# Performance work log

Hardware: AMD Instinct MI355X
Metric: run time of the kernel (lower is better)

## Reference

```python
import jax, jax.numpy as jnp
import numpy as np

N_NODES = 50000
N_EDGES = 800000
D_IN = 100
HID = 128
N_LAYERS = 3
N_GRAPHS = 64


def setup_inputs() -> dict:
    key = jax.random.key(0)
    ks = jax.random.split(key, 10)
    x = jax.random.normal(ks[0], (N_NODES, D_IN), dtype=jnp.float32)
    edge_index = jax.random.randint(ks[1], (2, N_EDGES), 0, N_NODES, dtype=jnp.int64)
    batch = jnp.sort(jax.random.randint(ks[2], (N_NODES,), 0, N_GRAPHS, dtype=jnp.int64))
    s = 1.0 / np.sqrt(D_IN)
    W_enc = jax.random.uniform(ks[3], (D_IN, HID), jnp.float32, -s, s)
    b_enc = jax.random.uniform(ks[4], (HID,), jnp.float32, -s, s)
    sh = 1.0 / np.sqrt(HID)
    gcn_W = jax.random.uniform(ks[5], (N_LAYERS, HID, HID), jnp.float32, -sh, sh)
    gcn_b = jax.random.uniform(ks[6], (N_LAYERS, HID), jnp.float32, -sh, sh)
    W_reg = jax.random.uniform(ks[7], (HID, 1), jnp.float32, -sh, sh)
    b_reg = jax.random.uniform(ks[8], (1,), jnp.float32, -sh, sh)
    return {"x": x, "edge_index": edge_index, "batch": batch,
            "W_enc": W_enc, "b_enc": b_enc, "gcn_W": gcn_W, "gcn_b": gcn_b,
            "W_reg": W_reg, "b_reg": b_reg}


def reference(x, edge_index, batch, W_enc, b_enc, gcn_W, gcn_b, W_reg, b_reg):
    N = x.shape[0]
    # node encoder
    h = x @ W_enc + b_enc  # [N, HID]
    # GCN normalization with self-loops (edge_weight = 1, PyG gcn_norm)
    loop = jnp.arange(N, dtype=edge_index.dtype)
    src = jnp.concatenate([edge_index[0], loop])  # [E+N]
    dst = jnp.concatenate([edge_index[1], loop])
    deg = jax.ops.segment_sum(jnp.ones_like(src, dtype=h.dtype), dst, num_segments=N)
    dinv = jnp.where(deg > 0, jax.lax.rsqrt(deg), 0.0)
    norm = dinv[src] * dinv[dst]  # [E+N]
    for i in range(N_LAYERS):
        m = (h @ gcn_W[i])[src] * norm[:, None]           # gather + scale messages
        h = jax.ops.segment_sum(m, dst, num_segments=N)   # scatter-add aggregate
        h = jax.nn.relu(h + gcn_b[i])
    # global mean pool over graphs
    sums = jax.ops.segment_sum(h, batch, num_segments=N_GRAPHS)
    cnt = jax.ops.segment_sum(jnp.ones((N,), dtype=h.dtype), batch, num_segments=N_GRAPHS)
    pooled = sums / jnp.maximum(cnt, 1.0)[:, None]        # [N_GRAPHS, HID]
    return pooled @ W_reg + b_reg                         # [N_GRAPHS, 1]
```

## Files before the change

kernel.cpp:

```cpp
#include <hip/hip_runtime.h>
#include <hip/hip_fp16.h>

#define N_NODES 50000
#define N_EDGES 800000
#define D_INN 100
#define HID 128
#define N_GRAPHS 64
#define NBLK ((N_NODES + 255) / 256)
#define POOL_ROWS 128
#define POOL_BLOCKS ((N_NODES + POOL_ROWS - 1) / POOL_ROWS)

#define NBUCK 8
#define NODES_PER_BUCK (N_NODES / NBUCK)
#define SCAT_BLOCKS 2048
#define GEMM_BLOCKS 512
#define N_CHUNK (N_NODES / 16)

typedef _Float16 f16x8 __attribute__((ext_vector_type(8)));
typedef _Float16 f16x4 __attribute__((ext_vector_type(4)));
typedef float f32x4 __attribute__((ext_vector_type(4)));

__global__ __launch_bounds__(256) void k_setup(int* __restrict__ deg,
                                               float* __restrict__ sums,
                                               const float* __restrict__ W,
                                               const float* __restrict__ We,
                                               __half* __restrict__ Wt,
                                               __half* __restrict__ Wte) {
    int i = blockIdx.x * 256 + threadIdx.x;
    if (i < N_NODES) deg[i] = 1;
    if (i < N_GRAPHS * HID) sums[i] = 0.f;
    if (i < 3 * HID * HID) {
        int l = i >> 14, rem = i & 16383;
        int c = rem >> 7, k = rem & 127;
        Wt[(l << 14) + c * HID + k] = __float2half(W[(l << 14) + k * HID + c]);
    } else if (i < 4 * HID * HID) {
        int j = i - 3 * HID * HID;
        int c = j >> 7, k = j & 127;
        float v = (k < D_INN) ? We[k * HID + c] : 0.f;
        Wte[c * HID + k] = __float2half(v);
    }
}

__global__ __launch_bounds__(256) void k_deg(const int* __restrict__ dst,
                                             int* __restrict__ deg) {
    int b = blockIdx.x & (NBUCK - 1);
    int lo = b * NODES_PER_BUCK, hi = lo + NODES_PER_BUCK;
    int sub = blockIdx.x >> 3, nsub = gridDim.x >> 3;
    for (int e = sub * 256 + threadIdx.x; e < N_EDGES; e += nsub * 256) {
        int d = dst[e];
        if (d >= lo && d < hi) atomicAdd(&deg[d], 1);
    }
}

__global__ __launch_bounds__(256) void k_scan1(const int* __restrict__ deg,
                                               int* __restrict__ incl,
                                               int* __restrict__ bsums) {
    __shared__ int sm[256];
    int i = blockIdx.x * 256 + threadIdx.x;
    int v = (i < N_NODES) ? deg[i] : 0;
    sm[threadIdx.x] = v;
    __syncthreads();
    for (int off = 1; off < 256; off <<= 1) {
        int t = (threadIdx.x >= off) ? sm[threadIdx.x - off] : 0;
        __syncthreads();
        sm[threadIdx.x] += t;
        __syncthreads();
    }
    if (i < N_NODES) incl[i] = sm[threadIdx.x];
    if (threadIdx.x == 255) bsums[blockIdx.x] = sm[255];
}

__global__ __launch_bounds__(256) void k_scan2(const int* __restrict__ bsums,
                                               int* __restrict__ boff) {
    __shared__ int sm[256];
    int v = (threadIdx.x < NBLK) ? bsums[threadIdx.x] : 0;
    sm[threadIdx.x] = v;
    __syncthreads();
    for (int off = 1; off < 256; off <<= 1) {
        int t = (threadIdx.x >= off) ? sm[threadIdx.x - off] : 0;
        __syncthreads();
        sm[threadIdx.x] += t;
        __syncthreads();
    }
    boff[threadIdx.x] = sm[threadIdx.x] - v;
}

__global__ void k_scan3(const int* __restrict__ incl, const int* __restrict__ boff,
                        const int* __restrict__ deg, int* __restrict__ offsets,
                        int* __restrict__ cursor, int* __restrict__ csr_src,
                        float* __restrict__ dinv) {
    int i = blockIdx.x * 256 + threadIdx.x;
    if (i < N_NODES) {
        int off1 = incl[i] + boff[blockIdx.x];
        offsets[i + 1] = off1;
        int dg = deg[i];
        int p0 = off1 - dg;
        csr_src[p0] = i;
        cursor[i] = p0 + 1;
        dinv[i] = rsqrtf((float)dg);
    }
    if (i == 0) offsets[0] = 0;
}

__global__ __launch_bounds__(256) void k_fill(const int* __restrict__ src,
                                              const int* __restrict__ dst,
                                              int* __restrict__ cursor,
                                              int* __restrict__ csr_src) {
    int b = blockIdx.x & (NBUCK - 1);
    int lo = b * NODES_PER_BUCK, hi = lo + NODES_PER_BUCK;
    int sub = blockIdx.x >> 3, nsub = gridDim.x >> 3;
    for (int e = sub * 256 + threadIdx.x; e < N_EDGES; e += nsub * 256) {
        int d = dst[e];
        if (d >= lo && d < hi) {
            int s = src[e];
            int p = atomicAdd(&cursor[d], 1);
            csr_src[p] = s;
        }
    }
}

__global__ __launch_bounds__(256) void k_genc(const float* __restrict__ x,
                                              const _Float16* __restrict__ Wt,
                                              const float* __restrict__ bias,
                                              _Float16* __restrict__ out) {
    const int lane = threadIdx.x & 63;
    const int wave = threadIdx.x >> 6;
    const int l15  = lane & 15;
    const int lhi  = lane >> 4;
    f16x8 wf0[4], wf1[4];
#pragma unroll
    for (int ks = 0; ks < 4; ++ks) {
        wf0[ks] = *(const f16x8*)(Wt + (wave * 32 + l15) * HID + ks * 32 + lhi * 8);
        wf1[ks] = *(const f16x8*)(Wt + (wave * 32 + 16 + l15) * HID + ks * 32 + lhi * 8);
    }
    f32x4 bq0 = ((const f32x4*)bias)[wave * 8 + lhi];
    f32x4 bq1 = ((const f32x4*)bias)[wave * 8 + 4 + lhi];
    for (int chunk = blockIdx.x; chunk < N_CHUNK; chunk += gridDim.x) {
        int row0 = chunk * 16;
        const float* xr = x + (row0 + l15) * D_INN + lhi * 8;
        f16x8 nf[4];
#pragma unroll
        for (int ks = 0; ks < 3; ++ks) {
            float4 a = *(const float4*)(xr + ks * 32);
            float4 b = *(const float4*)(xr + ks * 32 + 4);
            f16x8 t;
            t[0] = (_Float16)a.x; t[1] = (_Float16)a.y;
            t[2] = (_Float16)a.z; t[3] = (_Float16)a.w;
            t[4] = (_Float16)b.x; t[5] = (_Float16)b.y;
            t[6] = (_Float16)b.z; t[7] = (_Float16)b.w;
            nf[ks] = t;
        }
        {
            f16x8 t;
            int kb = 96 + lhi * 8;
#pragma unroll
            for (int j = 0; j < 8; ++j)
                t[j] = (kb + j < D_INN) ? (_Float16)xr[96 + j] : (_Float16)0.f;
            nf[3] = t;
        }
        f32x4 acc0 = {0.f, 0.f, 0.f, 0.f};
        f32x4 acc1 = {0.f, 0.f, 0.f, 0.f};
#pragma unroll
        for (int ks = 0; ks < 4; ++ks) {
            acc0 = __builtin_amdgcn_mfma_f32_16x16x32_f16(wf0[ks], nf[ks], acc0, 0, 0, 0);
            acc1 = __builtin_amdgcn_mfma_f32_16x16x32_f16(wf1[ks], nf[ks], acc1, 0, 0, 0);
        }
        int node = row0 + l15;
        f16x4 o0, o1;
#pragma unroll
        for (int r = 0; r < 4; ++r) {
            o0[r] = (_Float16)(acc0[r] + bq0[r]);
            o1[r] = (_Float16)(acc1[r] + bq1[r]);
        }
        *(f16x4*)(out + node * HID + wave * 32 + lhi * 4) = o0;
        *(f16x4*)(out + node * HID + wave * 32 + 16 + lhi * 4) = o1;
    }
}

__global__ __launch_bounds__(256) void k_gemm(const _Float16* __restrict__ A,
                                              const _Float16* __restrict__ Wt,
                                              const float* __restrict__ dinv,
                                              _Float16* __restrict__ out) {
    const int lane = threadIdx.x & 63;
    const int wave = threadIdx.x >> 6;
    const int l15  = lane & 15;
    const int lhi  = lane >> 4;
    f16x8 wf0[4], wf1[4];
#pragma unroll
    for (int ks = 0; ks < 4; ++ks) {
        wf0[ks] = *(const f16x8*)(Wt + (wave * 32 + l15) * HID + ks * 32 + lhi * 8);
        wf1[ks] = *(const f16x8*)(Wt + (wave * 32 + 16 + l15) * HID + ks * 32 + lhi * 8);
    }
    for (int chunk = blockIdx.x; chunk < N_CHUNK; chunk += gridDim.x) {
        int row0 = chunk * 16;
        const _Float16* Ar = A + (row0 + l15) * HID + lhi * 8;
        f16x8 nf0 = *(const f16x8*)(Ar);
        f16x8 nf1 = *(const f16x8*)(Ar + 32);
        f16x8 nf2 = *(const f16x8*)(Ar + 64);
        f16x8 nf3 = *(const f16x8*)(Ar + 96);
        f32x4 acc0 = {0.f, 0.f, 0.f, 0.f};
        f32x4 acc1 = {0.f, 0.f, 0.f, 0.f};
        acc0 = __builtin_amdgcn_mfma_f32_16x16x32_f16(wf0[0], nf0, acc0, 0, 0, 0);
        acc1 = __builtin_amdgcn_mfma_f32_16x16x32_f16(wf1[0], nf0, acc1, 0, 0, 0);
        acc0 = __builtin_amdgcn_mfma_f32_16x16x32_f16(wf0[1], nf1, acc0, 0, 0, 0);
        acc1 = __builtin_amdgcn_mfma_f32_16x16x32_f16(wf1[1], nf1, acc1, 0, 0, 0);
        acc0 = __builtin_amdgcn_mfma_f32_16x16x32_f16(wf0[2], nf2, acc0, 0, 0, 0);
        acc1 = __builtin_amdgcn_mfma_f32_16x16x32_f16(wf1[2], nf2, acc1, 0, 0, 0);
        acc0 = __builtin_amdgcn_mfma_f32_16x16x32_f16(wf0[3], nf3, acc0, 0, 0, 0);
        acc1 = __builtin_amdgcn_mfma_f32_16x16x32_f16(wf1[3], nf3, acc1, 0, 0, 0);
        int node = row0 + l15;
        float dr = dinv[node];
        f16x4 o0, o1;
#pragma unroll
        for (int r = 0; r < 4; ++r) {
            o0[r] = (_Float16)(acc0[r] * dr);
            o1[r] = (_Float16)(acc1[r] * dr);
        }
        *(f16x4*)(out + node * HID + wave * 32 + lhi * 4) = o0;
        *(f16x4*)(out + node * HID + wave * 32 + 16 + lhi * 4) = o1;
    }
}

__global__ __launch_bounds__(256) void k_agg(const __half* __restrict__ B,
                                             const int* __restrict__ offsets,
                                             const int* __restrict__ csr_src,
                                             const float* __restrict__ dinv,
                                             const float* __restrict__ bias,
                                             __half* __restrict__ A) {
    int node = (blockIdx.x * 256 + threadIdx.x) >> 6;
    int lane = threadIdx.x & 63;
    if (node >= N_NODES) return;
    int beg = offsets[node], end = offsets[node + 1];
    float ax0 = 0.f, ay0 = 0.f, ax1 = 0.f, ay1 = 0.f;
    const __half2* B2 = (const __half2*)B;
    int j = beg;
    while (j < end) {
        int take = end - j; if (take > 64) take = 64;
        int s_l = (lane < take) ? csr_src[j + lane] : 0;
        int t = 0;
        for (; t + 8 <= take; t += 8) {
            int s0 = __shfl(s_l, t + 0), s1 = __shfl(s_l, t + 1);
            int s2 = __shfl(s_l, t + 2), s3 = __shfl(s_l, t + 3);
            int s4 = __shfl(s_l, t + 4), s5 = __shfl(s_l, t + 5);
            int s6 = __shfl(s_l, t + 6), s7 = __shfl(s_l, t + 7);
            __half2 v0 = B2[s0 * 64 + lane];
            __half2 v1 = B2[s1 * 64 + lane];
            __half2 v2 = B2[s2 * 64 + lane];
            __half2 v3 = B2[s3 * 64 + lane];
            __half2 v4 = B2[s4 * 64 + lane];
            __half2 v5 = B2[s5 * 64 + lane];
            __half2 v6 = B2[s6 * 64 + lane];
            __half2 v7 = B2[s7 * 64 + lane];
            float2 f0 = __half22float2(v0);
            float2 f1 = __half22float2(v1);
            float2 f2 = __half22float2(v2);
            float2 f3 = __half22float2(v3);
            float2 f4 = __half22float2(v4);
            float2 f5 = __half22float2(v5);
            float2 f6 = __half22float2(v6);
            float2 f7 = __half22float2(v7);
            ax0 += f0.x; ay0 += f0.y;
            ax1 += f1.x; ay1 += f1.y;
            ax0 += f2.x; ay0 += f2.y;
            ax1 += f3.x; ay1 += f3.y;
            ax0 += f4.x; ay0 += f4.y;
            ax1 += f5.x; ay1 += f5.y;
            ax0 += f6.x; ay0 += f6.y;
            ax1 += f7.x; ay1 += f7.y;
        }
        for (; t + 4 <= take; t += 4) {
            int s0 = __shfl(s_l, t + 0), s1 = __shfl(s_l, t + 1);
            int s2 = __shfl(s_l, t + 2), s3 = __shfl(s_l, t + 3);
            float2 f0 = __half22float2(B2[s0 * 64 + lane]);
            float2 f1 = __half22float2(B2[s1 * 64 + lane]);
            float2 f2 = __half22float2(B2[s2 * 64 + lane]);
            float2 f3 = __half22float2(B2[s3 * 64 + lane]);
            ax0 += f0.x; ay0 += f0.y;
            ax1 += f1.x; ay1 += f1.y;
            ax0 += f2.x; ay0 += f2.y;
            ax1 += f3.x; ay1 += f3.y;
        }
        for (; t < take; ++t) {
            int s = __shfl(s_l, t);
            float2 f = __half22float2(B2[s * 64 + lane]);
            ax0 += f.x; ay0 += f.y;
        }
        j += take;
    }
    float dn = dinv[node];
    float2 b = ((const float2*)bias)[lane];
    float rx = fmaxf(fmaf(dn, ax0 + ax1, b.x), 0.f);
    float ry = fmaxf(fmaf(dn, ay0 + ay1, b.y), 0.f);
    ((__half2*)A)[node * 64 + lane] = __floats2half2_rn(rx, ry);
}

__global__ __launch_bounds__(64) void k_pool_part(const __half* __restrict__ A,
                                                  const int* __restrict__ batch,
                                                  float* __restrict__ sums) {
    int base = blockIdx.x * POOL_ROWS;
    if (base >= N_NODES) return;
    int c = threadIdx.x;
    int end = base + POOL_ROWS;
    if (end > N_NODES) end = N_NODES;
    const __half2* A2 = (const __half2*)A;
    float ax = 0.f, ay = 0.f;
    int g = batch[base];
    for (int n = base; n < end; ++n) {
        int bg = batch[n];
        if (bg != g) {
            atomicAdd(&sums[g * HID + 2 * c], ax);
            atomicAdd(&sums[g * HID + 2 * c + 1], ay);
            ax = 0.f; ay = 0.f;
            g = bg;
        }
        float2 f = __half22float2(A2[n * 64 + c]);
        ax += f.x; ay += f.y;
    }
    atomicAdd(&sums[g * HID + 2 * c], ax);
    atomicAdd(&sums[g * HID + 2 * c + 1], ay);
}

__global__ __launch_bounds__(128) void k_head(const float* __restrict__ sums,
                                              const int* __restrict__ batch,
                                              const float* __restrict__ W_reg,
                                              const float* __restrict__ b_reg,
                                              float* __restrict__ out) {
    int g = blockIdx.x;
    int lo = 0, hi = N_NODES;
    while (lo < hi) { int mid = (lo + hi) >> 1; if (batch[mid] < g) lo = mid + 1; else hi = mid; }
    int start = lo;
    hi = N_NODES;
    while (lo < hi) { int mid = (lo + hi) >> 1; if (batch[mid] < g + 1) lo = mid + 1; else hi = mid; }
    int end = lo;
    float cnt = (float)((end - start) > 0 ? (end - start) : 1);
    float v = (sums[g * HID + threadIdx.x] / cnt) * W_reg[threadIdx.x];
    for (int off = 32; off > 0; off >>= 1) v += __shfl_down(v, off);
    __shared__ float sm[2];
    if ((threadIdx.x & 63) == 0) sm[threadIdx.x >> 6] = v;
    __syncthreads();
    if (threadIdx.x == 0) out[g] = sm[0] + sm[1] + b_reg[0];
}

extern "C" void kernel_launch(void* const* d_in, const int* in_sizes, int n_in,
                              void* d_out, int out_size, void* d_ws, size_t ws_size,
                              hipStream_t stream) {
    const float* x      = (const float*)d_in[0];
    const int*   e_src  = (const int*)d_in[1];
    const int*   e_dst  = e_src + N_EDGES;
    const int*   batch  = (const int*)d_in[2];
    const float* W_enc  = (const float*)d_in[3];
    const float* b_enc  = (const float*)d_in[4];
    const float* gcn_W  = (const float*)d_in[5];
    const float* gcn_b  = (const float*)d_in[6];
    const float* W_reg  = (const float*)d_in[7];
    const float* b_reg  = (const float*)d_in[8];
    float* out = (float*)d_out;

    char* p = (char*)d_ws;
    auto carve = [&](size_t bytes) { char* q = p; p += (bytes + 255) & ~(size_t)255; return q; };
    __half* hA      = (__half*)carve(sizeof(__half) * N_NODES * HID);
    __half* msg     = (__half*)carve(sizeof(__half) * N_NODES * HID);
    __half* Wt      = (__half*)carve(sizeof(__half) * 3 * HID * HID);
    __half* Wte     = (__half*)carve(sizeof(__half) * HID * HID);
    int*    csr_src = (int*)   carve(sizeof(int)    * (N_EDGES + N_NODES));
    int*    deg     = (int*)   carve(sizeof(int)    * N_NODES);
    int*    cursor  = (int*)   carve(sizeof(int)    * N_NODES);
    int*    offsets = (int*)   carve(sizeof(int)    * (N_NODES + 1));
    int*    incl    = (int*)   carve(sizeof(int)    * N_NODES);
    int*    bsums   = (int*)   carve(sizeof(int)    * 256);
    int*    boff    = (int*)   carve(sizeof(int)    * 256);
    float*  dinv    = (float*) carve(sizeof(float)  * N_NODES);
    float*  sums    = (float*) carve(sizeof(float)  * N_GRAPHS * HID);

    k_setup<<<256, 256, 0, stream>>>(deg, sums, gcn_W, W_enc, Wt, Wte);
    k_deg<<<SCAT_BLOCKS, 256, 0, stream>>>(e_dst, deg);
    k_scan1<<<NBLK, 256, 0, stream>>>(deg, incl, bsums);
    k_scan2<<<1, 256, 0, stream>>>(bsums, boff);
    k_scan3<<<NBLK, 256, 0, stream>>>(incl, boff, deg, offsets, cursor, csr_src, dinv);
    k_fill<<<SCAT_BLOCKS, 256, 0, stream>>>(e_src, e_dst, cursor, csr_src);

    k_genc<<<GEMM_BLOCKS, 256, 0, stream>>>(
        x, (const _Float16*)Wte, b_enc, (_Float16*)hA);
    for (int l = 0; l < 3; ++l) {
        k_gemm<<<GEMM_BLOCKS, 256, 0, stream>>>(
            (const _Float16*)hA, (const _Float16*)(Wt + l * HID * HID), dinv,
            (_Float16*)msg);
        k_agg<<<(N_NODES * 64 + 255) / 256, 256, 0, stream>>>(
            msg, offsets, csr_src, dinv, gcn_b + l * HID, hA);
    }
    k_pool_part<<<POOL_BLOCKS, 64, 0, stream>>>(hA, batch, sums);
    k_head<<<N_GRAPHS, 128, 0, stream>>>(sums, batch, W_reg, b_reg, out);
}
```

Measured before the change: 360.7 us.

## Split node features into four column-block planes for cache-friendly aggregation

Stores the hidden features as four separate planes of 32 columns each, so [4][N][32] replaces [N][128]. The GEMM, encoder, aggregation and pooling kernels are all changed to match. The aggregation grid gets four times as many blocks, each handling one column quarter, so every block gathers from a quarter-sized table that fits better in L2/MALL. Each wave now reads 4 neighbor rows at a time with 64-byte segments and reduces across lane groups with shuffles. The cost is four passes over the CSR indices and smaller, less coalesced gather segments.

Result: slower. 440.8 us (+22.2%).

```diff
diff --git a/kernel.cpp b/kernel.cpp
--- a/kernel.cpp
+++ b/kernel.cpp
@@ -15,6 +15,9 @@
 #define SCAT_BLOCKS 2048
 #define GEMM_BLOCKS 512
 #define N_CHUNK (N_NODES / 16)
+
+#define CB4_STRIDE  (N_NODES * 32)
+#define CB4_STRIDE2 (N_NODES * 16)
 
 typedef _Float16 f16x8 __attribute__((ext_vector_type(8)));
 typedef _Float16 f16x4 __attribute__((ext_vector_type(4)));
@@ -172,8 +175,8 @@
             o0[r] = (_Float16)(acc0[r] + bq0[r]);
             o1[r] = (_Float16)(acc1[r] + bq1[r]);
         }
-        *(f16x4*)(out + node * HID + wave * 32 + lhi * 4) = o0;
-        *(f16x4*)(out + node * HID + wave * 32 + 16 + lhi * 4) = o1;
+        *(f16x4*)(out + wave * CB4_STRIDE + node * 32 + lhi * 4) = o0;
+        *(f16x4*)(out + wave * CB4_STRIDE + node * 32 + 16 + lhi * 4) = o1;
     }
 }
 
@@ -193,11 +196,11 @@
     }
     for (int chunk = blockIdx.x; chunk < N_CHUNK; chunk += gridDim.x) {
         int row0 = chunk * 16;
-        const _Float16* Ar = A + (row0 + l15) * HID + lhi * 8;
+        const _Float16* Ar = A + (row0 + l15) * 32 + lhi * 8;
         f16x8 nf0 = *(const f16x8*)(Ar);
-        f16x8 nf1 = *(const f16x8*)(Ar + 32);
-        f16x8 nf2 = *(const f16x8*)(Ar + 64);
-        f16x8 nf3 = *(const f16x8*)(Ar + 96);
+        f16x8 nf1 = *(const f16x8*)(Ar + CB4_STRIDE);
+        f16x8 nf2 = *(const f16x8*)(Ar + 2 * CB4_STRIDE);
+        f16x8 nf3 = *(const f16x8*)(Ar + 3 * CB4_STRIDE);
         f32x4 acc0 = {0.f, 0.f, 0.f, 0.f};
         f32x4 acc1 = {0.f, 0.f, 0.f, 0.f};
         acc0 = __builtin_amdgcn_mfma_f32_16x16x32_f16(wf0[0], nf0, acc0, 0, 0, 0);
@@ -216,108 +219,92 @@
             o0[r] = (_Float16)(acc0[r] * dr);
             o1[r] = (_Float16)(acc1[r] * dr);
         }
-        *(f16x4*)(out + node * HID + wave * 32 + lhi * 4) = o0;
-        *(f16x4*)(out + node * HID + wave * 32 + 16 + lhi * 4) = o1;
-    }
-}
-
-__global__ __launch_bounds__(256) void k_agg(const __half* __restrict__ B,
+        *(f16x4*)(out + wave * CB4_STRIDE + node * 32 + lhi * 4) = o0;
+        *(f16x4*)(out + wave * CB4_STRIDE + node * 32 + 16 + lhi * 4) = o1;
+    }
+}
+
+__global__ __launch_bounds__(256) void k_agg(const __half2* __restrict__ B2,
                                              const int* __restrict__ offsets,
                                              const int* __restrict__ csr_src,
                                              const float* __restrict__ dinv,
                                              const float* __restrict__ bias,
-                                             __half* __restrict__ A) {
-    int node = (blockIdx.x * 256 + threadIdx.x) >> 6;
+                                             __half2* __restrict__ A2) {
+    int q = blockIdx.x & 3;
+    int node = (blockIdx.x >> 2) * 4 + (threadIdx.x >> 6);
     int lane = threadIdx.x & 63;
-    if (node >= N_NODES) return;
+    int col = lane & 15;
+    int grp = lane >> 4;
+    const __half2* Bq = B2 + q * CB4_STRIDE2;
     int beg = offsets[node], end = offsets[node + 1];
     float ax0 = 0.f, ay0 = 0.f, ax1 = 0.f, ay1 = 0.f;
-    const __half2* B2 = (const __half2*)B;
     int j = beg;
     while (j < end) {
         int take = end - j; if (take > 64) take = 64;
         int s_l = (lane < take) ? csr_src[j + lane] : 0;
         int t = 0;
-        for (; t + 8 <= take; t += 8) {
-            int s0 = __shfl(s_l, t + 0), s1 = __shfl(s_l, t + 1);
-            int s2 = __shfl(s_l, t + 2), s3 = __shfl(s_l, t + 3);
-            int s4 = __shfl(s_l, t + 4), s5 = __shfl(s_l, t + 5);
-            int s6 = __shfl(s_l, t + 6), s7 = __shfl(s_l, t + 7);
-            __half2 v0 = B2[s0 * 64 + lane];
-            __half2 v1 = B2[s1 * 64 + lane];
-            __half2 v2 = B2[s2 * 64 + lane];
-            __half2 v3 = B2[s3 * 64 + lane];
-            __half2 v4 = B2[s4 * 64 + lane];
-            __half2 v5 = B2[s5 * 64 + lane];
-            __half2 v6 = B2[s6 * 64 + lane];
-            __half2 v7 = B2[s7 * 64 + lane];
-            float2 f0 = __half22float2(v0);
-            float2 f1 = __half22float2(v1);
-            float2 f2 = __half22float2(v2);
-            float2 f3 = __half22float2(v3);
-            float2 f4 = __half22float2(v4);
-            float2 f5 = __half22float2(v5);
-            float2 f6 = __half22float2(v6);
-            float2 f7 = __half22float2(v7);
-            ax0 += f0.x; ay0 += f0.y;
-            ax1 += f1.x; ay1 += f1.y;
-            ax0 += f2.x; ay0 += f2.y;
-            ax1 += f3.x; ay1 += f3.y;
-            ax0 += f4.x; ay0 += f4.y;
-            ax1 += f5.x; ay1 += f5.y;
-            ax0 += f6.x; ay0 += f6.y;
-            ax1 += f7.x; ay1 += f7.y;
-        }
-        for (; t + 4 <= take; t += 4) {
-            int s0 = __shfl(s_l, t + 0), s1 = __shfl(s_l, t + 1);
-            int s2 = __shfl(s_l, t + 2), s3 = __shfl(s_l, t + 3);
-            float2 f0 = __half22float2(B2[s0 * 64 + lane]);
-            float2 f1 = __half22float2(B2[s1 * 64 + lane]);
-            float2 f2 = __half22float2(B2[s2 * 64 + lane]);
-            float2 f3 = __half22float2(B2[s3 * 64 + lane]);
-            ax0 += f0.x; ay0 += f0.y;
-            ax1 += f1.x; ay1 += f1.y;
-            ax0 += f2.x; ay0 += f2.y;
-            ax1 += f3.x; ay1 += f3.y;
-        }
-        for (; t < take; ++t) {
-            int s = __shfl(s_l, t);
-            float2 f = __half22float2(B2[s * 64 + lane]);
-            ax0 += f.x; ay0 += f.y;
+        for (; t + 16 <= take; t += 16) {
+            int sa = __shfl(s_l, t +  0 + grp);
+            int sb = __shfl(s_l, t +  4 + grp);
+            int sc = __shfl(s_l, t +  8 + grp);
+            int sd = __shfl(s_l, t + 12 + grp);
+            float2 fa = __half22float2(Bq[sa * 16 + col]);
+            float2 fb = __half22float2(Bq[sb * 16 + col]);
+            float2 fc = __half22float2(Bq[sc * 16 + col]);
+            float2 fd = __half22float2(Bq[sd * 16 + col]);
+            ax0 += fa.x; ay0 += fa.y;
+            ax1 += fb.x; ay1 += fb.y;
+            ax0 += fc.x; ay0 += fc.y;
+            ax1 += fd.x; ay1 += fd.y;
+        }
+        for (; t < take; t += 4) {
+            int idx = t + grp;
+            int si = __shfl(s_l, idx < take ? idx : 0);
+            if (idx < take) {
+                float2 f = __half22float2(Bq[si * 16 + col]);
+                ax0 += f.x; ay0 += f.y;
+            }
         }
         j += take;
     }
-    float dn = dinv[node];
-    float2 b = ((const float2*)bias)[lane];
-    float rx = fmaxf(fmaf(dn, ax0 + ax1, b.x), 0.f);
-    float ry = fmaxf(fmaf(dn, ay0 + ay1, b.y), 0.f);
-    ((__half2*)A)[node * 64 + lane] = __floats2half2_rn(rx, ry);
-}
-
-__global__ __launch_bounds__(64) void k_pool_part(const __half* __restrict__ A,
+    float ax = ax0 + ax1, ay = ay0 + ay1;
+    ax += __shfl_xor(ax, 16); ay += __shfl_xor(ay, 16);
+    ax += __shfl_xor(ax, 32); ay += __shfl_xor(ay, 32);
+    if (lane < 16) {
+        float dn = dinv[node];
+        int cg = q * 32 + col * 2;
+        float rx = fmaxf(fmaf(dn, ax, bias[cg]), 0.f);
+        float ry = fmaxf(fmaf(dn, ay, bias[cg + 1]), 0.f);
+        A2[q * CB4_STRIDE2 + node * 16 + col] = __floats2half2_rn(rx, ry);
+    }
+}
+
+__global__ __launch_bounds__(64) void k_pool_part(const __half2* __restrict__ A2,
                                                   const int* __restrict__ batch,
                                                   float* __restrict__ sums) {
     int base = blockIdx.x * POOL_ROWS;
     if (base >= N_NODES) return;
-    int c = threadIdx.x;
+    int c2 = threadIdx.x;
+    int q = c2 >> 4, off = c2 & 15;
+    int cg = q * 32 + off * 2;
+    const __half2* Aq = A2 + q * CB4_STRIDE2;
     int end = base + POOL_ROWS;
     if (end > N_NODES) end = N_NODES;
-    const __half2* A2 = (const __half2*)A;
     float ax = 0.f, ay = 0.f;
     int g = batch[base];
     for (int n = base; n < end; ++n) {
         int bg = batch[n];
         if (bg != g) {
-            atomicAdd(&sums[g * HID + 2 * c], ax);
-            atomicAdd(&sums[g * HID + 2 * c + 1], ay);
+            atomicAdd(&sums[g * HID + cg], ax);
+            atomicAdd(&sums[g * HID + cg + 1], ay);
             ax = 0.f; ay = 0.f;
             g = bg;
         }
-        float2 f = __half22float2(A2[n * 64 + c]);
+        float2 f = __half22float2(Aq[n * 16 + off]);
         ax += f.x; ay += f.y;
     }
-    atomicAdd(&sums[g * HID + 2 * c], ax);
-    atomicAdd(&sums[g * HID + 2 * c + 1], ay);
+    atomicAdd(&sums[g * HID + cg], ax);
+    atomicAdd(&sums[g * HID + cg + 1], ay);
 }
 
 __global__ __launch_bounds__(128) void k_head(const float* __restrict__ sums,
@@ -385,9 +372,10 @@
         k_gemm<<<GEMM_BLOCKS, 256, 0, stream>>>(
             (const _Float16*)hA, (const _Float16*)(Wt + l * HID * HID), dinv,
             (_Float16*)msg);
-        k_agg<<<(N_NODES * 64 + 255) / 256, 256, 0, stream>>>(
-            msg, offsets, csr_src, dinv, gcn_b + l * HID, hA);
-    }
-    k_pool_part<<<POOL_BLOCKS, 64, 0, stream>>>(hA, batch, sums);
+        k_agg<<<N_NODES, 256, 0, stream>>>(
+            (const __half2*)msg, offsets, csr_src, dinv, gcn_b + l * HID,
+            (__half2*)hA);
+    }
+    k_pool_part<<<POOL_BLOCKS, 64, 0, stream>>>((const __half2*)hA, batch, sums);
     k_head<<<N_GRAPHS, 128, 0, stream>>>(sums, batch, W_reg, b_reg, out);
 }
```
